# Kernel optimization log

Measured on AMD Instinct MI355X. Metric: run time of the kernel, lower is better.

Reference implementation:

```python
import jax, jax.numpy as jnp
import numpy as np
from jax import lax

FEAT_X, FEAT_Y = 50, 37          # generate_anchors(50, 37)
BASE_SIZE, DSR = 8.0, 16.0
A = FEAT_X * FEAT_Y * 9          # 16650 anchors


def generate_anchors():
    # Vectorized version of the triple python loop; order: x, y, size, [b1,b2,b3]
    xs = jnp.arange(FEAT_X, dtype=jnp.float32)[:, None, None]
    ys = jnp.arange(FEAT_Y, dtype=jnp.float32)[None, :, None]
    s = jnp.array([BASE_SIZE, 2 * BASE_SIZE, 4 * BASE_SIZE], jnp.float32)[None, None, :]

    def box(x1, y1, x2, y2):
        return jnp.stack(jnp.broadcast_arrays(x1 * DSR, y1 * DSR, x2 * DSR, y2 * DSR), axis=-1)

    b1 = box(xs - s / 2, ys - s / 2, xs + s / 2, ys + s / 2)      # square
    b2 = box(xs - s,     ys - s / 4, xs + s,     ys + s / 4)      # wide
    b3 = box(xs - s / 4, ys - s,     xs + s / 4, ys + s)          # tall
    anchors = jnp.stack([b1, b2, b3], axis=3)  # (50,37,3 sizes,3 variants,4)
    return anchors.reshape(-1, 4)              # (16650,4)


def conv2d(x, w, b, padding):
    y = lax.conv_general_dilated(x, w, (1, 1), padding,
                                 dimension_numbers=("NCHW", "OIHW", "NCHW"))
    return y + b[None, :, None, None]


def pairwise_iou(anchors, gt):
    # anchors: (A,4), gt: (B,G,4) -> iou (B,A,G); zero when no positive overlap
    a = anchors[None, :, None, :]
    g = gt[:, None, :, :]
    area_a = (a[..., 2] - a[..., 0]) * (a[..., 3] - a[..., 1])
    area_g = (g[..., 2] - g[..., 0]) * (g[..., 3] - g[..., 1])
    left = jnp.maximum(a[..., 0], g[..., 0])
    right = jnp.minimum(a[..., 2], g[..., 2])
    top = jnp.maximum(a[..., 1], g[..., 1])
    bot = jnp.minimum(a[..., 3], g[..., 3])
    no_ov = (left >= right) | (top >= bot)
    inter = jnp.where(no_ov, 0.0, (right - left) * (bot - top))
    return jnp.where(no_ov, 0.0, inter / (area_a + area_g - inter))


def setup_inputs() -> dict:
    key = jax.random.key(0)
    k1, k2, k3, k4, k5, k6, k7, k8 = jax.random.split(key, 8)
    B, G = 8, 20
    feats = jax.random.normal(k1, (B, 512, FEAT_Y, FEAT_X), jnp.float32)
    # well-formed gt boxes inside an ~800x592 image
    raw = jax.random.uniform(k2, (B, G, 2, 2)) * jnp.array([800.0, 592.0])
    x1y1 = jnp.min(raw, axis=2)
    x2y2 = jnp.max(raw, axis=2) + 1.0
    gt_boxes = jnp.concatenate([x1y1, x2y2], axis=-1)  # (B,G,4)
    im_info = jnp.array([[592.0, 800.0, 1.0]], jnp.float32)  # (h, w, scale)
    s = 0.02
    w3 = jax.random.normal(k3, (512, 512, 3, 3), jnp.float32) * s
    b3 = jnp.zeros((512,), jnp.float32)
    wc = jax.random.normal(k4, (18, 512, 1, 1), jnp.float32) * s
    bc = jnp.zeros((18,), jnp.float32)
    wb = jax.random.normal(k5, (36, 512, 1, 1), jnp.float32) * s
    bb = jnp.zeros((36,), jnp.float32)
    return {"feats": feats, "w3": w3, "b3": b3, "wc": wc, "bc": bc,
            "wb": wb, "bb": bb, "gt_boxes": gt_boxes, "im_info": im_info}


def reference(feats, w3, b3, wc, bc, wb, bb, gt_boxes, im_info):
    B = feats.shape[0]
    anchors = generate_anchors()
    rpn_conv1 = jax.nn.relu(conv2d(feats, w3, b3, ((1, 1), (1, 1))))
    rpn_cls_score = conv2d(rpn_conv1, wc, bc, ((0, 0), (0, 0)))  # (B,18,H,W)
    Bc, C, H, W = rpn_cls_score.shape
    score_rs = rpn_cls_score.reshape(Bc, 2, (C * H) // 2, W)      # reshape(x, 2)
    rpn_cls_prob = jax.nn.softmax(score_rs, axis=1).reshape(Bc, 18, H, W)
    rpn_bbox_pred = conv2d(rpn_conv1, wb, bb, ((0, 0), (0, 0)))   # (B,36,H,W)

    # anchor-target assignment (training branch), faithful to original logic
    inside = ((anchors[:, 0] >= 0) & (anchors[:, 1] >= 0) &
              (anchors[:, 2] < im_info[0, 1]) & (anchors[:, 3] < im_info[0, 0]))
    iou = pairwise_iou(anchors, gt_boxes)                 # (B,A,G)
    iou = jnp.where(inside[None, :, None], iou, 0.0)      # outside anchors skipped
    G = gt_boxes.shape[1]
    # original: idxs = argmax(iou_matrix[:][j]) with j == last gt index
    idx = jnp.argmax(iou[:, G - 1, :], axis=-1)           # (B,)
    labels = jnp.zeros((B, anchors.shape[0]), jnp.float32)
    labels = labels.at[jnp.arange(B), idx].set(1.0)
    max_iou = jnp.max(iou, axis=-1)                       # (B,A)
    labels = jnp.where(inside[None, :] & (max_iou > 0.7), 0.0, labels)

    out = jnp.concatenate([rpn_cls_prob, rpn_bbox_pred], axis=1)  # (B,54,H,W)
    return out, iou, labels
```

## Files before the change

### kernel.cpp

```cpp
#include <hip/hip_runtime.h>

typedef unsigned short u16;
typedef unsigned int u32;
typedef float f32x4 __attribute__((ext_vector_type(4)));
typedef short bf16x8 __attribute__((ext_vector_type(8)));

#define NB 8
#define FH 37
#define FW 50
#define FHW 1850
#define MTOT 14800
#define CIN 512
#define KTOT 4608
#define HP 39
#define WP 52
#define ANCH 16650
#define NG 20

#define ZB 356
#define WTB 512
#define WHB 128
#define TRB 3712
#define PRE_TOT (ZB + WTB + WHB + TRB)

#define CONVB 960
#define IOB 528

__device__ __forceinline__ u16 f2bf(float f) {
    u32 u = __float_as_uint(f);
    u += 0x7fffu + ((u >> 16) & 1u);
    return (u16)(u >> 16);
}

__device__ __forceinline__ void gl2lds16(const u16* g, u16* l) {
    __builtin_amdgcn_global_load_lds((const __attribute__((address_space(1))) void*)(g),
                                     (__attribute__((address_space(3))) void*)(l),
                                     16, 0, 0);
}

__device__ __forceinline__ void anchor_box(int a, float& x1, float& y1, float& x2, float& y2) {
    int x = a / 333;
    int rem = a - x * 333;
    int y = rem / 9;
    int r2 = rem - y * 9;
    int si = r2 / 3;
    int bi = r2 - si * 3;
    float s = (float)(8 << si);
    float fx = (float)x, fy = (float)y;
    float ax1, ay1, ax2, ay2;
    if (bi == 0)      { float h = s * 0.5f;  ax1 = fx - h; ay1 = fy - h; ax2 = fx + h; ay2 = fy + h; }
    else if (bi == 1) { float q = s * 0.25f; ax1 = fx - s; ay1 = fy - q; ax2 = fx + s; ay2 = fy + q; }
    else              { float q = s * 0.25f; ax1 = fx - q; ay1 = fy - s; ax2 = fx + q; ay2 = fy + s; }
    x1 = ax1 * 16.f; y1 = ay1 * 16.f; x2 = ax2 * 16.f; y2 = ay2 * 16.f;
}

__global__ __launch_bounds__(256) void k_pre(u16* __restrict__ apad,
                                             const float* __restrict__ w3, u16* __restrict__ wt,
                                             const float* __restrict__ wc, const float* __restrict__ wb,
                                             u16* __restrict__ whd,
                                             const float* __restrict__ feats) {
    __shared__ __attribute__((aligned(16))) char smraw[18432];
    int blk = blockIdx.x;
    int t = threadIdx.x;

    if (blk < ZB) {
        uint4* apad4 = (uint4*)apad;
        int i = blk * 256 + t;
        int img = i / 11392;
        int r = i - img * 11392;
        int u4;
        if (r < 3328) u4 = r;
        else if (r < 6656) u4 = 126464 + (r - 3328);
        else {
            int rp = r - 6656;
            int h = 1 + (rp >> 7);
            int c2 = rp & 127;
            int col = (c2 & 64) ? 51 : 0;
            u4 = (h * 52 + col) * 64 + (c2 & 63);
        }
        apad4[img * 129792 + u4] = make_uint4(0u, 0u, 0u, 0u);
    } else if (blk < ZB + WTB) {
        float* lt = (float*)smraw;
        int n = blk - ZB;
        const float* src = w3 + n * KTOT;
        for (int i = t; i < KTOT; i += 256) lt[i] = src[i];
        __syncthreads();
        u16* dst = wt + n * KTOT;
        for (int o = t; o < KTOT; o += 256) {
            int tap = o >> 9, ci = o & 511;
            dst[o] = f2bf(lt[ci * 9 + tap]);
        }
    } else if (blk < ZB + WTB + WHB) {
        int i = (blk - ZB - WTB) * 256 + t;
        int n = i >> 9;
        int ci = i & 511;
        float v = 0.f;
        if (n < 18) v = wc[n * 512 + ci];
        else if (n < 54) v = wb[(n - 18) * 512 + ci];
        whd[i] = f2bf(v);
    } else {
        float* tile = (float*)smraw;
        int q = blk - ZB - WTB - WHB;
        int xt = q % 58;
        int r2 = q / 58;
        int ct = r2 & 7;
        int img = r2 >> 3;
        int hw0 = xt * 32, c0 = ct * 64;
        int lx = t & 31, ly = t >> 5;
        #pragma unroll
        for (int rr = 0; rr < 8; rr++) {
            int cl = ly + rr * 8;
            int hw = hw0 + lx;
            if (hw < FHW) tile[cl * 33 + lx] = feats[(img * 512 + c0 + cl) * FHW + hw];
        }
        __syncthreads();
        #pragma unroll
        for (int rr = 0; rr < 4; rr++) {
            int hwl = ly + rr * 8;
            int hw2 = hw0 + hwl;
            if (hw2 < FHW) {
                int h = hw2 / FW, w = hw2 - h * FW;
                float v0 = tile[(2 * lx) * 33 + hwl];
                float v1 = tile[(2 * lx + 1) * 33 + hwl];
                u32 pk = (u32)f2bf(v0) | ((u32)f2bf(v1) << 16);
                u32* dst = (u32*)&apad[(((img * HP) + h + 1) * WP + (w + 1)) * 512 + c0];
                dst[lx] = pk;
            }
        }
    }
}

__global__ __launch_bounds__(256) void k_conv(const u16* __restrict__ apad,
                                              const u16* __restrict__ wt,
                                              const float* __restrict__ b3,
                                              u16* __restrict__ act,
                                              const float* __restrict__ gt,
                                              const float* __restrict__ im,
                                              float* __restrict__ iou_out,
                                              float* __restrict__ lab) {
    __shared__ __attribute__((aligned(16))) char sm[24576];
    __shared__ int idxs;
    int L = blockIdx.x;
    int tid = threadIdx.x;

    if (L < CONVB) {
        u16* As = (u16*)sm;
        u16* Bs = (u16*)(sm + 16384);
        int mb = (L & 7) + 8 * (L >> 6);
        int nb = (L >> 3) & 7;
        if (mb >= 116) return;
        int wave = tid >> 6, lane = tid & 63;
        int m0 = mb * 128;
        int n0 = nb * 64;
        int wr = wave >> 1, wn = wave & 1;
        int lm = lane & 15, lq = lane >> 4;
        int l7 = lm & 7;

        f32x4 acc[4][2] = {};

        int rloc = tid >> 3;
        int cg = (tid & 7) ^ (rloc & 7);
        int aBase[4], bBase[2];
        for (int i = 0; i < 4; i++) {
            int m = m0 + i * 32 + rloc; if (m > MTOT - 1) m = MTOT - 1;
            int b = m / FHW; int hw = m - b * FHW;
            int h = hw / FW; int w = hw - h * FW;
            aBase[i] = ((b * HP + h) * WP + w) * 512 + cg * 8;
        }
        for (int j = 0; j < 2; j++)
            bBase[j] = (n0 + j * 32 + rloc) * KTOT + cg * 8;

        u16* aL[4]; u16* bL[2];
        for (int i = 0; i < 4; i++) aL[i] = &As[(i * 32 + wave * 8) * 64];
        for (int j = 0; j < 2; j++) bL[j] = &Bs[(j * 32 + wave * 8) * 64];

        for (int kk = 0; kk < KTOT; kk += 64) {
            int tap = kk >> 9;
            int ci0 = kk & 511;
            int dy = tap / 3, dx = tap - dy * 3;
            int aOfs = (dy * WP + dx) * 512 + ci0;
            gl2lds16(apad + aBase[0] + aOfs, aL[0]);
            gl2lds16(apad + aBase[1] + aOfs, aL[1]);
            gl2lds16(apad + aBase[2] + aOfs, aL[2]);
            gl2lds16(apad + aBase[3] + aOfs, aL[3]);
            gl2lds16(wt + bBase[0] + kk, bL[0]);
            gl2lds16(wt + bBase[1] + kk, bL[1]);
            __syncthreads();
            bf16x8 a[2][4], b[2][2];
            #pragma unroll
            for (int ks = 0; ks < 2; ks++) {
                int slotb = ((ks * 4 + lq) ^ l7) * 8;
                #pragma unroll
                for (int i = 0; i < 4; i++)
                    a[ks][i] = *(const bf16x8*)&As[(wr * 64 + i * 16 + lm) * 64 + slotb];
                #pragma unroll
                for (int j = 0; j < 2; j++)
                    b[ks][j] = *(const bf16x8*)&Bs[(wn * 32 + j * 16 + lm) * 64 + slotb];
            }
            #pragma unroll
            for (int ks = 0; ks < 2; ks++)
                #pragma unroll
                for (int i = 0; i < 4; i++)
                    #pragma unroll
                    for (int j = 0; j < 2; j++)
                        acc[i][j] = __builtin_amdgcn_mfma_f32_16x16x32_bf16(a[ks][i], b[ks][j], acc[i][j], 0, 0, 0);
            __syncthreads();
        }

        for (int j = 0; j < 2; j++) {
            int n = n0 + wn * 32 + j * 16 + lm;
            float bias = b3[n];
            for (int i = 0; i < 4; i++) {
                int mb2 = m0 + wr * 64 + i * 16 + lq * 4;
                for (int r = 0; r < 4; r++) {
                    int m = mb2 + r;
                    if (m < MTOT) {
                        float v = acc[i][j][r] + bias;
                        act[m * 512 + n] = f2bf(v > 0.f ? v : 0.f);
                    }
                }
            }
        }
    } else {
        float* g4 = (float*)sm;
        float* imv = g4 + 80;
        float* buf = g4 + 84;
        int q = L - CONVB;
        int at = q % 66;
        int b = q / 66;
        int t = tid;
        if (t < NG * 4) g4[t] = gt[b * NG * 4 + t];
        if (t < 2) imv[t] = im[t];
        __syncthreads();
        if (t == 0) {
            float x1, y1, x2, y2;
            anchor_box(19, x1, y1, x2, y2);
            bool inside = (x1 >= 0.f) && (y1 >= 0.f) && (x2 < imv[1]) && (y2 < imv[0]);
            float aa = (x2 - x1) * (y2 - y1);
            float best = -1.f; int bg = 0;
            for (int g2 = 0; g2 < NG; g2++) {
                float gx1 = g4[g2 * 4], gy1 = g4[g2 * 4 + 1], gx2 = g4[g2 * 4 + 2], gy2 = g4[g2 * 4 + 3];
                float l = fmaxf(x1, gx1), r = fminf(x2, gx2);
                float tp = fmaxf(y1, gy1), bo = fminf(y2, gy2);
                float v = 0.f;
                if (l < r && tp < bo) {
                    float inter = (r - l) * (bo - tp);
                    float ag = (gx2 - gx1) * (gy2 - gy1);
                    v = inter / (aa + ag - inter);
                }
                if (!inside) v = 0.f;
                if (v > best) { best = v; bg = g2; }
            }
            idxs = bg;
        }
        int a0 = at * 256;
        int a = a0 + t;
        float mx = 0.f;
        bool inside = false;
        if (a < ANCH) {
            float x1, y1, x2, y2;
            anchor_box(a, x1, y1, x2, y2);
            inside = (x1 >= 0.f) && (y1 >= 0.f) && (x2 < imv[1]) && (y2 < imv[0]);
            float aa = (x2 - x1) * (y2 - y1);
            for (int g2 = 0; g2 < NG; g2++) {
                float gx1 = g4[g2 * 4], gy1 = g4[g2 * 4 + 1], gx2 = g4[g2 * 4 + 2], gy2 = g4[g2 * 4 + 3];
                float l = fmaxf(x1, gx1), r = fminf(x2, gx2);
                float tp = fmaxf(y1, gy1), bo = fminf(y2, gy2);
                float v = 0.f;
                if (l < r && tp < bo) {
                    float inter = (r - l) * (bo - tp);
                    float ag = (gx2 - gx1) * (gy2 - gy1);
                    v = inter / (aa + ag - inter);
                }
                if (!inside) v = 0.f;
                buf[t * NG + g2] = v;
                mx = fmaxf(mx, v);
            }
        }
        __syncthreads();
        int rem = ANCH - a0;
        int cnt2 = (rem < 256 ? rem : 256) * NG;
        float* dst = iou_out + (b * ANCH + a0) * NG;
        for (int i = t; i < cnt2; i += 256) dst[i] = buf[i];
        if (a < ANCH) {
            float lv = (a == idxs) ? 1.f : 0.f;
            if (inside && mx > 0.7f) lv = 0.f;
            lab[b * ANCH + a] = lv;
        }
    }
}

__global__ __launch_bounds__(256) void k_post(const u16* __restrict__ act,
                                              const u16* __restrict__ whd,
                                              const float* __restrict__ bc,
                                              const float* __restrict__ bb,
                                              float* __restrict__ out) {
    __shared__ float Sl[4 * 16 * 65];
    int tid = threadIdx.x;
    int wave = tid >> 6, lane = tid & 63;
    int lm = lane & 15, lq = lane >> 4;
    int m0 = blockIdx.x * 64 + wave * 16;
    int mr = m0 + lm; if (mr > MTOT - 1) mr = MTOT - 1;
    const u16* arow = act + mr * 512;
    f32x4 acc[4] = {};
    for (int kk = 0; kk < 512; kk += 32) {
        bf16x8 a = *(const bf16x8*)&arow[kk + lq * 8];
        #pragma unroll
        for (int j = 0; j < 4; j++) {
            bf16x8 b = *(const bf16x8*)&whd[(j * 16 + lm) * 512 + kk + lq * 8];
            acc[j] = __builtin_amdgcn_mfma_f32_16x16x32_bf16(a, b, acc[j], 0, 0, 0);
        }
    }
    float* S = &Sl[wave * 1040];
    #pragma unroll
    for (int r = 0; r < 4; r++)
        #pragma unroll
        for (int j = 0; j < 4; j++)
            S[(lq * 4 + r) * 65 + j * 16 + lm] = acc[j][r];
    __syncthreads();
    int r16 = lane & 15, cg = lane >> 4;
    int m = m0 + r16;
    if (m < MTOT) {
        int b = m / FHW, hw = m - b * FHW;
        const float* Sr = &S[r16 * 65];
        #pragma unroll
        for (int k = 0; k < 14; k++) {
            int c = cg + 4 * k;
            if (c >= 54) break;
            float v;
            if (c < 18) {
                int c0 = c < 9 ? c : c - 9;
                float s0 = Sr[c0] + bc[c0];
                float s1 = Sr[c0 + 9] + bc[c0 + 9];
                float mx = fmaxf(s0, s1);
                float e0 = __expf(s0 - mx), e1 = __expf(s1 - mx);
                v = (c < 9 ? e0 : e1) / (e0 + e1);
            } else {
                v = Sr[c] + bb[c - 18];
            }
            out[(b * 54 + c) * FHW + hw] = v;
        }
    }
}

extern "C" void kernel_launch(void* const* d_in, const int* in_sizes, int n_in,
                              void* d_out, int out_size, void* d_ws, size_t ws_size,
                              hipStream_t stream) {
    (void)in_sizes; (void)n_in; (void)out_size; (void)ws_size;
    const float* feats = (const float*)d_in[0];
    const float* w3    = (const float*)d_in[1];
    const float* b3    = (const float*)d_in[2];
    const float* wc    = (const float*)d_in[3];
    const float* bc    = (const float*)d_in[4];
    const float* wb    = (const float*)d_in[5];
    const float* bb    = (const float*)d_in[6];
    const float* gt    = (const float*)d_in[7];
    const float* im    = (const float*)d_in[8];
    float* out = (float*)d_out;
    char* ws = (char*)d_ws;

    u16* apad = (u16*)(ws);
    u16* wt   = (u16*)(ws + 16613376);
    u16* whd  = (u16*)(ws + 21331968);
    u16* act  = (u16*)(ws + 21397504);

    float* iou_out = out + 799200;
    float* lab     = out + 3463200;

    k_pre<<<dim3(PRE_TOT), dim3(256), 0, stream>>>(apad, w3, wt, wc, wb, whd, feats);
    k_conv<<<dim3(CONVB + IOB), dim3(256), 0, stream>>>(apad, wt, b3, act, gt, im, iou_out, lab);
    k_post<<<dim3(232), dim3(256), 0, stream>>>(act, whd, bc, bb, out);
}
```

Measured before the change: 202.6 us.

## Double-buffer LDS tiles in conv GEMM to overlap loads with MFMA

```diff
diff --git a/kernel.cpp b/kernel.cpp
--- a/kernel.cpp
+++ b/kernel.cpp
@@ -138,14 +138,16 @@
                                               const float* __restrict__ im,
                                               float* __restrict__ iou_out,
                                               float* __restrict__ lab) {
-    __shared__ __attribute__((aligned(16))) char sm[24576];
+    __shared__ __attribute__((aligned(16))) char sm[49152];
     __shared__ int idxs;
     int L = blockIdx.x;
     int tid = threadIdx.x;
 
     if (L < CONVB) {
-        u16* As = (u16*)sm;
-        u16* Bs = (u16*)(sm + 16384);
+        u16* A0 = (u16*)sm;
+        u16* B0 = A0 + 8192;
+        u16* A1 = (u16*)(sm + 24576);
+        u16* B1 = A1 + 8192;
         int mb = (L & 7) + 8 * (L >> 6);
         int nb = (L >> 3) & 7;
         if (mb >= 116) return;
@@ -170,42 +172,60 @@
         for (int j = 0; j < 2; j++)
             bBase[j] = (n0 + j * 32 + rloc) * KTOT + cg * 8;
 
-        u16* aL[4]; u16* bL[2];
-        for (int i = 0; i < 4; i++) aL[i] = &As[(i * 32 + wave * 8) * 64];
-        for (int j = 0; j < 2; j++) bL[j] = &Bs[(j * 32 + wave * 8) * 64];
-
-        for (int kk = 0; kk < KTOT; kk += 64) {
-            int tap = kk >> 9;
-            int ci0 = kk & 511;
-            int dy = tap / 3, dx = tap - dy * 3;
-            int aOfs = (dy * WP + dx) * 512 + ci0;
-            gl2lds16(apad + aBase[0] + aOfs, aL[0]);
-            gl2lds16(apad + aBase[1] + aOfs, aL[1]);
-            gl2lds16(apad + aBase[2] + aOfs, aL[2]);
-            gl2lds16(apad + aBase[3] + aOfs, aL[3]);
-            gl2lds16(wt + bBase[0] + kk, bL[0]);
-            gl2lds16(wt + bBase[1] + kk, bL[1]);
+        int aOff0 = wave * 512;
+        int aOff1 = 2048 + wave * 512;
+        int aOff2 = 4096 + wave * 512;
+        int aOff3 = 6144 + wave * 512;
+        int bOff0 = wave * 512;
+        int bOff1 = 2048 + wave * 512;
+
+#define STAGE(Abuf, Bbuf, KK) do {                                         \
+            int tap_ = (KK) >> 9;                                          \
+            int ci0_ = (KK) & 511;                                         \
+            int dy_ = tap_ / 3, dx_ = tap_ - dy_ * 3;                      \
+            int aOfs_ = (dy_ * WP + dx_) * 512 + ci0_;                     \
+            gl2lds16(apad + aBase[0] + aOfs_, (Abuf) + aOff0);             \
+            gl2lds16(apad + aBase[1] + aOfs_, (Abuf) + aOff1);             \
+            gl2lds16(apad + aBase[2] + aOfs_, (Abuf) + aOff2);             \
+            gl2lds16(apad + aBase[3] + aOfs_, (Abuf) + aOff3);             \
+            gl2lds16(wt + bBase[0] + (KK), (Bbuf) + bOff0);                \
+            gl2lds16(wt + bBase[1] + (KK), (Bbuf) + bOff1);                \
+        } while (0)
+
+#define COMPUTE(Abuf, Bbuf) do {                                           \
+            bf16x8 a_[2][4], b_[2][2];                                     \
+            _Pragma("unroll")                                              \
+            for (int ks = 0; ks < 2; ks++) {                               \
+                int slotb = ((ks * 4 + lq) ^ l7) * 8;                      \
+                _Pragma("unroll")                                          \
+                for (int i = 0; i < 4; i++)                                \
+                    a_[ks][i] = *(const bf16x8*)&(Abuf)[(wr * 64 + i * 16 + lm) * 64 + slotb]; \
+                _Pragma("unroll")                                          \
+                for (int j = 0; j < 2; j++)                                \
+                    b_[ks][j] = *(const bf16x8*)&(Bbuf)[(wn * 32 + j * 16 + lm) * 64 + slotb]; \
+            }                                                              \
+            _Pragma("unroll")                                              \
+            for (int ks = 0; ks < 2; ks++)                                 \
+                _Pragma("unroll")                                          \
+                for (int i = 0; i < 4; i++)                                \
+                    _Pragma("unroll")                                      \
+                    for (int j = 0; j < 2; j++)                            \
+                        acc[i][j] = __builtin_amdgcn_mfma_f32_16x16x32_bf16(a_[ks][i], b_[ks][j], acc[i][j], 0, 0, 0); \
+        } while (0)
+
+        STAGE(A0, B0, 0);
+        __syncthreads();
+
+        for (int kk = 0; kk < KTOT; kk += 128) {
+            STAGE(A1, B1, kk + 64);
+            COMPUTE(A0, B0);
             __syncthreads();
-            bf16x8 a[2][4], b[2][2];
-            #pragma unroll
-            for (int ks = 0; ks < 2; ks++) {
-                int slotb = ((ks * 4 + lq) ^ l7) * 8;
-                #pragma unroll
-                for (int i = 0; i < 4; i++)
-                    a[ks][i] = *(const bf16x8*)&As[(wr * 64 + i * 16 + lm) * 64 + slotb];
-                #pragma unroll
-                for (int j = 0; j < 2; j++)
-                    b[ks][j] = *(const bf16x8*)&Bs[(wn * 32 + j * 16 + lm) * 64 + slotb];
-            }
-            #pragma unroll
-            for (int ks = 0; ks < 2; ks++)
-                #pragma unroll
-                for (int i = 0; i < 4; i++)
-                    #pragma unroll
-                    for (int j = 0; j < 2; j++)
-                        acc[i][j] = __builtin_amdgcn_mfma_f32_16x16x32_bf16(a[ks][i], b[ks][j], acc[i][j], 0, 0, 0);
+            if (kk + 128 < KTOT) STAGE(A0, B0, kk + 128);
+            COMPUTE(A1, B1);
             __syncthreads();
         }
+#undef STAGE
+#undef COMPUTE
 
         for (int j = 0; j < 2; j++) {
             int n = n0 + wn * 32 + j * 16 + lm;
```

Result: slower. 229.1 us (+13.1%).

## Fuse three kernels into one persistent kernel with atomic grid barriers

Applied to the files above, without the earlier changes.

```diff
diff --git a/kernel.cpp b/kernel.cpp
--- a/kernel.cpp
+++ b/kernel.cpp
@@ -22,9 +22,13 @@
 #define WHB 128
 #define TRB 3712
 #define PRE_TOT (ZB + WTB + WHB + TRB)
+#define IOB 528
+#define PREV_TOT (PRE_TOT + IOB)
 
 #define CONVB 960
-#define IOB 528
+#define POSTB 232
+
+#define GRID_ALL 960
 
 __device__ __forceinline__ u16 f2bf(float f) {
     u32 u = __float_as_uint(f);
@@ -36,6 +40,22 @@
     __builtin_amdgcn_global_load_lds((const __attribute__((address_space(1))) void*)(g),
                                      (__attribute__((address_space(3))) void*)(l),
                                      16, 0, 0);
+}
+
+__device__ __forceinline__ void grid_barrier(u32* ctr) {
+    __syncthreads();
+    if (threadIdx.x == 0) {
+        __threadfence();
+        atomicAdd(ctr, 1u);
+        int guard = 0;
+        while (__hip_atomic_load(ctr, __ATOMIC_ACQUIRE, __HIP_MEMORY_SCOPE_AGENT) < GRID_ALL
+               && guard < (1 << 21)) {
+            __builtin_amdgcn_s_sleep(8);
+            ++guard;
+        }
+        __threadfence();
+    }
+    __syncthreads();
 }
 
 __device__ __forceinline__ void anchor_box(int a, float& x1, float& y1, float& x2, float& y2) {
@@ -54,291 +74,294 @@
     x1 = ax1 * 16.f; y1 = ay1 * 16.f; x2 = ax2 * 16.f; y2 = ay2 * 16.f;
 }
 
-__global__ __launch_bounds__(256) void k_pre(u16* __restrict__ apad,
-                                             const float* __restrict__ w3, u16* __restrict__ wt,
-                                             const float* __restrict__ wc, const float* __restrict__ wb,
-                                             u16* __restrict__ whd,
-                                             const float* __restrict__ feats) {
-    __shared__ __attribute__((aligned(16))) char smraw[18432];
-    int blk = blockIdx.x;
-    int t = threadIdx.x;
-
-    if (blk < ZB) {
-        uint4* apad4 = (uint4*)apad;
-        int i = blk * 256 + t;
-        int img = i / 11392;
-        int r = i - img * 11392;
-        int u4;
-        if (r < 3328) u4 = r;
-        else if (r < 6656) u4 = 126464 + (r - 3328);
-        else {
-            int rp = r - 6656;
-            int h = 1 + (rp >> 7);
-            int c2 = rp & 127;
-            int col = (c2 & 64) ? 51 : 0;
-            u4 = (h * 52 + col) * 64 + (c2 & 63);
-        }
-        apad4[img * 129792 + u4] = make_uint4(0u, 0u, 0u, 0u);
-    } else if (blk < ZB + WTB) {
-        float* lt = (float*)smraw;
-        int n = blk - ZB;
-        const float* src = w3 + n * KTOT;
-        for (int i = t; i < KTOT; i += 256) lt[i] = src[i];
-        __syncthreads();
-        u16* dst = wt + n * KTOT;
-        for (int o = t; o < KTOT; o += 256) {
-            int tap = o >> 9, ci = o & 511;
-            dst[o] = f2bf(lt[ci * 9 + tap]);
-        }
-    } else if (blk < ZB + WTB + WHB) {
-        int i = (blk - ZB - WTB) * 256 + t;
-        int n = i >> 9;
-        int ci = i & 511;
-        float v = 0.f;
-        if (n < 18) v = wc[n * 512 + ci];
-        else if (n < 54) v = wb[(n - 18) * 512 + ci];
-        whd[i] = f2bf(v);
-    } else {
-        float* tile = (float*)smraw;
-        int q = blk - ZB - WTB - WHB;
-        int xt = q % 58;
-        int r2 = q / 58;
-        int ct = r2 & 7;
-        int img = r2 >> 3;
-        int hw0 = xt * 32, c0 = ct * 64;
-        int lx = t & 31, ly = t >> 5;
-        #pragma unroll
-        for (int rr = 0; rr < 8; rr++) {
-            int cl = ly + rr * 8;
-            int hw = hw0 + lx;
-            if (hw < FHW) tile[cl * 33 + lx] = feats[(img * 512 + c0 + cl) * FHW + hw];
+__global__ __launch_bounds__(256, 4) void k_all(u16* __restrict__ apad,
+                                                const float* __restrict__ w3, u16* __restrict__ wt,
+                                                const float* __restrict__ wc, const float* __restrict__ wb,
+                                                u16* __restrict__ whd,
+                                                const float* __restrict__ feats,
+                                                const float* __restrict__ b3,
+                                                u16* __restrict__ act,
+                                                const float* __restrict__ gt,
+                                                const float* __restrict__ im,
+                                                float* __restrict__ iou_out,
+                                                float* __restrict__ lab,
+                                                const float* __restrict__ bc,
+                                                const float* __restrict__ bb,
+                                                float* __restrict__ out,
+                                                u32* __restrict__ bar) {
+    __shared__ __attribute__((aligned(16))) char sm[24576];
+    __shared__ int idxs;
+    int tid = threadIdx.x;
+
+    for (int vb = blockIdx.x; vb < PREV_TOT; vb += GRID_ALL) {
+        if (vb < ZB) {
+            uint4* apad4 = (uint4*)apad;
+            int i = vb * 256 + tid;
+            int img = i / 11392;
+            int r = i - img * 11392;
+            int u4;
+            if (r < 3328) u4 = r;
+            else if (r < 6656) u4 = 126464 + (r - 3328);
+            else {
+                int rp = r - 6656;
+                int h = 1 + (rp >> 7);
+                int c2 = rp & 127;
+                int col = (c2 & 64) ? 51 : 0;
+                u4 = (h * 52 + col) * 64 + (c2 & 63);
+            }
+            apad4[img * 129792 + u4] = make_uint4(0u, 0u, 0u, 0u);
+        } else if (vb < ZB + WTB) {
+            float* lt = (float*)sm;
+            int n = vb - ZB;
+            const float* src = w3 + n * KTOT;
+            for (int i = tid; i < KTOT; i += 256) lt[i] = src[i];
+            __syncthreads();
+            u16* dst = wt + n * KTOT;
+            for (int o = tid; o < KTOT; o += 256) {
+                int tap = o >> 9, ci = o & 511;
+                dst[o] = f2bf(lt[ci * 9 + tap]);
+            }
+        } else if (vb < ZB + WTB + WHB) {
+            int i = (vb - ZB - WTB) * 256 + tid;
+            int n = i >> 9;
+            int ci = i & 511;
+            float v = 0.f;
+            if (n < 18) v = wc[n * 512 + ci];
+            else if (n < 54) v = wb[(n - 18) * 512 + ci];
+            if (n < 54) whd[i] = f2bf(v);
+        } else if (vb < PRE_TOT) {
+            float* tile = (float*)sm;
+            int q = vb - ZB - WTB - WHB;
+            int xt = q % 58;
+            int r2 = q / 58;
+            int ct = r2 & 7;
+            int img = r2 >> 3;
+            int hw0 = xt * 32, c0 = ct * 64;
+            int lx = tid & 31, ly = tid >> 5;
+            #pragma unroll
+            for (int rr = 0; rr < 8; rr++) {
+                int cl = ly + rr * 8;
+                int hw = hw0 + lx;
+                if (hw < FHW) tile[cl * 33 + lx] = feats[(img * 512 + c0 + cl) * FHW + hw];
+            }
+            __syncthreads();
+            #pragma unroll
+            for (int rr = 0; rr < 4; rr++) {
+                int hwl = ly + rr * 8;
+                int hw2 = hw0 + hwl;
+                if (hw2 < FHW) {
+                    int h = hw2 / FW, w = hw2 - h * FW;
+                    float v0 = tile[(2 * lx) * 33 + hwl];
+                    float v1 = tile[(2 * lx + 1) * 33 + hwl];
+                    u32 pk = (u32)f2bf(v0) | ((u32)f2bf(v1) << 16);
+                    u32* dst = (u32*)&apad[(((img * HP) + h + 1) * WP + (w + 1)) * 512 + c0];
+                    dst[lx] = pk;
+                }
+            }
+        } else {
+            float* g4 = (float*)sm;
+            float* imv = g4 + 80;
+            float* buf = g4 + 84;
+            int q = vb - PRE_TOT;
+            int at = q % 66;
+            int b = q / 66;
+            int t = tid;
+            if (t < NG * 4) g4[t] = gt[b * NG * 4 + t];
+            if (t < 2) imv[t] = im[t];
+            __syncthreads();
+            if (t == 0) {
+                float x1, y1, x2, y2;
+                anchor_box(19, x1, y1, x2, y2);
+                bool inside = (x1 >= 0.f) && (y1 >= 0.f) && (x2 < imv[1]) && (y2 < imv[0]);
+                float aa = (x2 - x1) * (y2 - y1);
+                float best = -1.f; int bg = 0;
+                for (int g2 = 0; g2 < NG; g2++) {
+                    float gx1 = g4[g2 * 4], gy1 = g4[g2 * 4 + 1], gx2 = g4[g2 * 4 + 2], gy2 = g4[g2 * 4 + 3];
+                    float l = fmaxf(x1, gx1), r = fminf(x2, gx2);
+                    float tp = fmaxf(y1, gy1), bo = fminf(y2, gy2);
+                    float v = 0.f;
+                    if (l < r && tp < bo) {
+                        float inter = (r - l) * (bo - tp);
+                        float ag = (gx2 - gx1) * (gy2 - gy1);
+                        v = inter / (aa + ag - inter);
+                    }
+                    if (!inside) v = 0.f;
+                    if (v > best) { best = v; bg = g2; }
+                }
+                idxs = bg;
+            }
+            int a0 = at * 256;
+            int a = a0 + t;
+            float mx = 0.f;
+            bool inside = false;
+            if (a < ANCH) {
+                float x1, y1, x2, y2;
+                anchor_box(a, x1, y1, x2, y2);
+                inside = (x1 >= 0.f) && (y1 >= 0.f) && (x2 < imv[1]) && (y2 < imv[0]);
+                float aa = (x2 - x1) * (y2 - y1);
+                for (int g2 = 0; g2 < NG; g2++) {
+                    float gx1 = g4[g2 * 4], gy1 = g4[g2 * 4 + 1], gx2 = g4[g2 * 4 + 2], gy2 = g4[g2 * 4 + 3];
+                    float l = fmaxf(x1, gx1), r = fminf(x2, gx2);
+                    float tp = fmaxf(y1, gy1), bo = fminf(y2, gy2);
+                    float v = 0.f;
+                    if (l < r && tp < bo) {
+                        float inter = (r - l) * (bo - tp);
+                        float ag = (gx2 - gx1) * (gy2 - gy1);
+                        v = inter / (aa + ag - inter);
+                    }
+                    if (!inside) v = 0.f;
+                    buf[t * NG + g2] = v;
+                    mx = fmaxf(mx, v);
+                }
+            }
+            __syncthreads();
+            int rem = ANCH - a0;
+            int cnt2 = (rem < 256 ? rem : 256) * NG;
+            float* dst = iou_out + (b * ANCH + a0) * NG;
+            for (int i = t; i < cnt2; i += 256) dst[i] = buf[i];
+            if (a < ANCH) {
+                float lv = (a == idxs) ? 1.f : 0.f;
+                if (inside && mx > 0.7f) lv = 0.f;
+                lab[b * ANCH + a] = lv;
+            }
         }
         __syncthreads();
-        #pragma unroll
-        for (int rr = 0; rr < 4; rr++) {
-            int hwl = ly + rr * 8;
-            int hw2 = hw0 + hwl;
-            if (hw2 < FHW) {
-                int h = hw2 / FW, w = hw2 - h * FW;
-                float v0 = tile[(2 * lx) * 33 + hwl];
-                float v1 = tile[(2 * lx + 1) * 33 + hwl];
-                u32 pk = (u32)f2bf(v0) | ((u32)f2bf(v1) << 16);
-                u32* dst = (u32*)&apad[(((img * HP) + h + 1) * WP + (w + 1)) * 512 + c0];
-                dst[lx] = pk;
-            }
-        }
     }
-}
-
-__global__ __launch_bounds__(256) void k_conv(const u16* __restrict__ apad,
-                                              const u16* __restrict__ wt,
-                                              const float* __restrict__ b3,
-                                              u16* __restrict__ act,
-                                              const float* __restrict__ gt,
-                                              const float* __restrict__ im,
-                                              float* __restrict__ iou_out,
-                                              float* __restrict__ lab) {
-    __shared__ __attribute__((aligned(16))) char sm[24576];
-    __shared__ int idxs;
-    int L = blockIdx.x;
-    int tid = threadIdx.x;
-
-    if (L < CONVB) {
+
+    grid_barrier(bar);
+
+    {
+        int L = blockIdx.x;
         u16* As = (u16*)sm;
         u16* Bs = (u16*)(sm + 16384);
         int mb = (L & 7) + 8 * (L >> 6);
         int nb = (L >> 3) & 7;
-        if (mb >= 116) return;
-        int wave = tid >> 6, lane = tid & 63;
-        int m0 = mb * 128;
-        int n0 = nb * 64;
-        int wr = wave >> 1, wn = wave & 1;
-        int lm = lane & 15, lq = lane >> 4;
-        int l7 = lm & 7;
-
-        f32x4 acc[4][2] = {};
-
-        int rloc = tid >> 3;
-        int cg = (tid & 7) ^ (rloc & 7);
-        int aBase[4], bBase[2];
-        for (int i = 0; i < 4; i++) {
-            int m = m0 + i * 32 + rloc; if (m > MTOT - 1) m = MTOT - 1;
-            int b = m / FHW; int hw = m - b * FHW;
-            int h = hw / FW; int w = hw - h * FW;
-            aBase[i] = ((b * HP + h) * WP + w) * 512 + cg * 8;
-        }
-        for (int j = 0; j < 2; j++)
-            bBase[j] = (n0 + j * 32 + rloc) * KTOT + cg * 8;
-
-        u16* aL[4]; u16* bL[2];
-        for (int i = 0; i < 4; i++) aL[i] = &As[(i * 32 + wave * 8) * 64];
-        for (int j = 0; j < 2; j++) bL[j] = &Bs[(j * 32 + wave * 8) * 64];
-
-        for (int kk = 0; kk < KTOT; kk += 64) {
-            int tap = kk >> 9;
-            int ci0 = kk & 511;
-            int dy = tap / 3, dx = tap - dy * 3;
-            int aOfs = (dy * WP + dx) * 512 + ci0;
-            gl2lds16(apad + aBase[0] + aOfs, aL[0]);
-            gl2lds16(apad + aBase[1] + aOfs, aL[1]);
-            gl2lds16(apad + aBase[2] + aOfs, aL[2]);
-            gl2lds16(apad + aBase[3] + aOfs, aL[3]);
-            gl2lds16(wt + bBase[0] + kk, bL[0]);
-            gl2lds16(wt + bBase[1] + kk, bL[1]);
-            __syncthreads();
-            bf16x8 a[2][4], b[2][2];
-            #pragma unroll
-            for (int ks = 0; ks < 2; ks++) {
-                int slotb = ((ks * 4 + lq) ^ l7) * 8;
-                #pragma unroll
-                for (int i = 0; i < 4; i++)
-                    a[ks][i] = *(const bf16x8*)&As[(wr * 64 + i * 16 + lm) * 64 + slotb];
-                #pragma unroll
-                for (int j = 0; j < 2; j++)
-                    b[ks][j] = *(const bf16x8*)&Bs[(wn * 32 + j * 16 + lm) * 64 + slotb];
-            }
-            #pragma unroll
-            for (int ks = 0; ks < 2; ks++)
-                #pragma unroll
-                for (int i = 0; i < 4; i++)
+        if (L < CONVB && mb < 116) {
+            int wave = tid >> 6, lane = tid & 63;
+            int m0 = mb * 128;
+            int n0 = nb * 64;
+            int wr = wave >> 1, wn = wave & 1;
+            int lm = lane & 15, lq = lane >> 4;
+            int l7 = lm & 7;
+
+            f32x4 acc[4][2] = {};
+
+            int rloc = tid >> 3;
+            int cg2 = (tid & 7) ^ (rloc & 7);
+            int aBase[4], bBase[2];
+            for (int i = 0; i < 4; i++) {
+                int m = m0 + i * 32 + rloc; if (m > MTOT - 1) m = MTOT - 1;
+                int b = m / FHW; int hw = m - b * FHW;
+                int h = hw / FW; int w = hw - h * FW;
+                aBase[i] = ((b * HP + h) * WP + w) * 512 + cg2 * 8;
+            }
+            for (int j = 0; j < 2; j++)
+                bBase[j] = (n0 + j * 32 + rloc) * KTOT + cg2 * 8;
+
+            u16* aL[4]; u16* bL[2];
+            for (int i = 0; i < 4; i++) aL[i] = &As[(i * 32 + wave * 8) * 64];
+            for (int j = 0; j < 2; j++) bL[j] = &Bs[(j * 32 + wave * 8) * 64];
+
+            for (int kk = 0; kk < KTOT; kk += 64) {
+                int tap = kk >> 9;
+                int ci0 = kk & 511;
+                int dy = tap / 3, dx = tap - dy * 3;
+                int aOfs = (dy * WP + dx) * 512 + ci0;
+                gl2lds16(apad + aBase[0] + aOfs, aL[0]);
+                gl2lds16(apad + aBase[1] + aOfs, aL[1]);
+                gl2lds16(apad + aBase[2] + aOfs, aL[2]);
+                gl2lds16(apad + aBase[3] + aOfs, aL[3]);
+                gl2lds16(wt + bBase[0] + kk, bL[0]);
+                gl2lds16(wt + bBase[1] + kk, bL[1]);
+                __syncthreads();
+                bf16x8 a[2][4], b[2][2];
+                #pragma unroll
+                for (int ks = 0; ks < 2; ks++) {
+                    int slotb = ((ks * 4 + lq) ^ l7) * 8;
+                    #pragma unroll
+                    for (int i = 0; i < 4; i++)
+                        a[ks][i] = *(const bf16x8*)&As[(wr * 64 + i * 16 + lm) * 64 + slotb];
                     #pragma unroll
                     for (int j = 0; j < 2; j++)
-                        acc[i][j] = __builtin_amdgcn_mfma_f32_16x16x32_bf16(a[ks][i], b[ks][j], acc[i][j], 0, 0, 0);
-            __syncthreads();
-        }
-
-        for (int j = 0; j < 2; j++) {
-            int n = n0 + wn * 32 + j * 16 + lm;
-            float bias = b3[n];
-            for (int i = 0; i < 4; i++) {
-                int mb2 = m0 + wr * 64 + i * 16 + lq * 4;
-                for (int r = 0; r < 4; r++) {
-                    int m = mb2 + r;
-                    if (m < MTOT) {
-                        float v = acc[i][j][r] + bias;
-                        act[m * 512 + n] = f2bf(v > 0.f ? v : 0.f);
+                        b[ks][j] = *(const bf16x8*)&Bs[(wn * 32 + j * 16 + lm) * 64 + slotb];
+                }
+                #pragma unroll
+                for (int ks = 0; ks < 2; ks++)
+                    #pragma unroll
+                    for (int i = 0; i < 4; i++)
+                        #pragma unroll
+                        for (int j = 0; j < 2; j++)
+                            acc[i][j] = __builtin_amdgcn_mfma_f32_16x16x32_bf16(a[ks][i], b[ks][j], acc[i][j], 0, 0, 0);
+                __syncthreads();
+            }
+
+            for (int j = 0; j < 2; j++) {
+                int n = n0 + wn * 32 + j * 16 + lm;
+                float bias = b3[n];
+                for (int i = 0; i < 4; i++) {
+                    int mb2 = m0 + wr * 64 + i * 16 + lq * 4;
+                    for (int r = 0; r < 4; r++) {
+                        int m = mb2 + r;
+                        if (m < MTOT) {
+                            float v = acc[i][j][r] + bias;
+                            act[m * 512 + n] = f2bf(v > 0.f ? v : 0.f);
+                        }
                     }
                 }
             }
-        }
-    } else {
-        float* g4 = (float*)sm;
-        float* imv = g4 + 80;
-        float* buf = g4 + 84;
-        int q = L - CONVB;
-        int at = q % 66;
-        int b = q / 66;
-        int t = tid;
-        if (t < NG * 4) g4[t] = gt[b * NG * 4 + t];
-        if (t < 2) imv[t] = im[t];
-        __syncthreads();
-        if (t == 0) {
-            float x1, y1, x2, y2;
-            anchor_box(19, x1, y1, x2, y2);
-            bool inside = (x1 >= 0.f) && (y1 >= 0.f) && (x2 < imv[1]) && (y2 < imv[0]);
-            float aa = (x2 - x1) * (y2 - y1);
-            float best = -1.f; int bg = 0;
-            for (int g2 = 0; g2 < NG; g2++) {
-                float gx1 = g4[g2 * 4], gy1 = g4[g2 * 4 + 1], gx2 = g4[g2 * 4 + 2], gy2 = g4[g2 * 4 + 3];
-                float l = fmaxf(x1, gx1), r = fminf(x2, gx2);
-                float tp = fmaxf(y1, gy1), bo = fminf(y2, gy2);
-                float v = 0.f;
-                if (l < r && tp < bo) {
-                    float inter = (r - l) * (bo - tp);
-                    float ag = (gx2 - gx1) * (gy2 - gy1);
-                    v = inter / (aa + ag - inter);
-                }
-                if (!inside) v = 0.f;
-                if (v > best) { best = v; bg = g2; }
-            }
-            idxs = bg;
-        }
-        int a0 = at * 256;
-        int a = a0 + t;
-        float mx = 0.f;
-        bool inside = false;
-        if (a < ANCH) {
-            float x1, y1, x2, y2;
-            anchor_box(a, x1, y1, x2, y2);
-            inside = (x1 >= 0.f) && (y1 >= 0.f) && (x2 < imv[1]) && (y2 < imv[0]);
-            float aa = (x2 - x1) * (y2 - y1);
-            for (int g2 = 0; g2 < NG; g2++) {
-                float gx1 = g4[g2 * 4], gy1 = g4[g2 * 4 + 1], gx2 = g4[g2 * 4 + 2], gy2 = g4[g2 * 4 + 3];
-                float l = fmaxf(x1, gx1), r = fminf(x2, gx2);
-                float tp = fmaxf(y1, gy1), bo = fminf(y2, gy2);
-                float v = 0.f;
-                if (l < r && tp < bo) {
-                    float inter = (r - l) * (bo - tp);
-                    float ag = (gx2 - gx1) * (gy2 - gy1);
-                    v = inter / (aa + ag - inter);
-                }
-                if (!inside) v = 0.f;
-                buf[t * NG + g2] = v;
-                mx = fmaxf(mx, v);
-            }
-        }
-        __syncthreads();
-        int rem = ANCH - a0;
-        int cnt2 = (rem < 256 ? rem : 256) * NG;
-        float* dst = iou_out + (b * ANCH + a0) * NG;
-        for (int i = t; i < cnt2; i += 256) dst[i] = buf[i];
-        if (a < ANCH) {
-            float lv = (a == idxs) ? 1.f : 0.f;
-            if (inside && mx > 0.7f) lv = 0.f;
-            lab[b * ANCH + a] = lv;
         }
     }
-}
-
-__global__ __launch_bounds__(256) void k_post(const u16* __restrict__ act,
-                                              const u16* __restrict__ whd,
-                                              const float* __restrict__ bc,
-                                              const float* __restrict__ bb,
-                                              float* __restrict__ out) {
-    __shared__ float Sl[4 * 16 * 65];
-    int tid = threadIdx.x;
-    int wave = tid >> 6, lane = tid & 63;
-    int lm = lane & 15, lq = lane >> 4;
-    int m0 = blockIdx.x * 64 + wave * 16;
-    int mr = m0 + lm; if (mr > MTOT - 1) mr = MTOT - 1;
-    const u16* arow = act + mr * 512;
-    f32x4 acc[4] = {};
-    for (int kk = 0; kk < 512; kk += 32) {
-        bf16x8 a = *(const bf16x8*)&arow[kk + lq * 8];
-        #pragma unroll
-        for (int j = 0; j < 4; j++) {
-            bf16x8 b = *(const bf16x8*)&whd[(j * 16 + lm) * 512 + kk + lq * 8];
-            acc[j] = __builtin_amdgcn_mfma_f32_16x16x32_bf16(a, b, acc[j], 0, 0, 0);
-        }
-    }
-    float* S = &Sl[wave * 1040];
-    #pragma unroll
-    for (int r = 0; r < 4; r++)
-        #pragma unroll
-        for (int j = 0; j < 4; j++)
-            S[(lq * 4 + r) * 65 + j * 16 + lm] = acc[j][r];
-    __syncthreads();
-    int r16 = lane & 15, cg = lane >> 4;
-    int m = m0 + r16;
-    if (m < MTOT) {
-        int b = m / FHW, hw = m - b * FHW;
-        const float* Sr = &S[r16 * 65];
-        #pragma unroll
-        for (int k = 0; k < 14; k++) {
-            int c = cg + 4 * k;
-            if (c >= 54) break;
-            float v;
-            if (c < 18) {
-                int c0 = c < 9 ? c : c - 9;
-                float s0 = Sr[c0] + bc[c0];
-                float s1 = Sr[c0 + 9] + bc[c0 + 9];
-                float mx = fmaxf(s0, s1);
-                float e0 = __expf(s0 - mx), e1 = __expf(s1 - mx);
-                v = (c < 9 ? e0 : e1) / (e0 + e1);
-            } else {
-                v = Sr[c] + bb[c - 18];
-            }
-            out[(b * 54 + c) * FHW + hw] = v;
+
+    grid_barrier(bar + 32);
+
+    {
+        int vb = blockIdx.x;
+        if (vb < POSTB) {
+            float* Sl = (float*)sm;
+            int wave = tid >> 6, lane = tid & 63;
+            int lm = lane & 15, lq = lane >> 4;
+            int m0 = vb * 64 + wave * 16;
+            int mr = m0 + lm; if (mr > MTOT - 1) mr = MTOT - 1;
+            const u16* arow = act + mr * 512;
+            f32x4 acc[4] = {};
+            for (int kk = 0; kk < 512; kk += 32) {
+                bf16x8 a = *(const bf16x8*)&arow[kk + lq * 8];
+                #pragma unroll
+                for (int j = 0; j < 4; j++) {
+                    bf16x8 b = *(const bf16x8*)&whd[(j * 16 + lm) * 512 + kk + lq * 8];
+                    acc[j] = __builtin_amdgcn_mfma_f32_16x16x32_bf16(a, b, acc[j], 0, 0, 0);
+                }
+            }
+            float* S = &Sl[wave * 1040];
+            #pragma unroll
+            for (int r = 0; r < 4; r++)
+                #pragma unroll
+                for (int j = 0; j < 4; j++)
+                    S[(lq * 4 + r) * 65 + j * 16 + lm] = acc[j][r];
+            __syncthreads();
+            int r16 = lane & 15, cg2 = lane >> 4;
+            int m = m0 + r16;
+            if (m < MTOT) {
+                int b = m / FHW, hw = m - b * FHW;
+                const float* Sr = &S[r16 * 65];
+                #pragma unroll
+                for (int k = 0; k < 14; k++) {
+                    int c = cg2 + 4 * k;
+                    if (c >= 54) break;
+                    float v;
+                    if (c < 18) {
+                        int c0 = c < 9 ? c : c - 9;
+                        float s0 = Sr[c0] + bc[c0];
+                        float s1 = Sr[c0 + 9] + bc[c0 + 9];
+                        float mx = fmaxf(s0, s1);
+                        float e0 = __expf(s0 - mx), e1 = __expf(s1 - mx);
+                        v = (c < 9 ? e0 : e1) / (e0 + e1);
+                    } else {
+                        v = Sr[c] + bb[c - 18];
+                    }
+                    out[(b * 54 + c) * FHW + hw] = v;
+                }
+            }
         }
     }
 }
@@ -364,10 +387,13 @@
     u16* whd  = (u16*)(ws + 21331968);
     u16* act  = (u16*)(ws + 21397504);
 
+    u32* bar = (u32*)(ws + 21331968 + 55296);
+
     float* iou_out = out + 799200;
     float* lab     = out + 3463200;
 
-    k_pre<<<dim3(PRE_TOT), dim3(256), 0, stream>>>(apad, w3, wt, wc, wb, whd, feats);
-    k_conv<<<dim3(CONVB + IOB), dim3(256), 0, stream>>>(apad, wt, b3, act, gt, im, iou_out, lab);
-    k_post<<<dim3(232), dim3(256), 0, stream>>>(act, whd, bc, bb, out);
-}
+    hipMemsetAsync(bar, 0, 256, stream);
+    k_all<<<dim3(GRID_ALL), dim3(256), 0, stream>>>(apad, w3, wt, wc, wb, whd,
+                                                    feats, b3, act, gt, im,
+                                                    iou_out, lab, bc, bb, out, bar);
+}
```

Result: slower. 807.5 us (+298.6%).
